# Optimization experiments

Hardware: AMD Instinct MI355X
Metric: run time of the kernel (lower is better)

## Reference

```python
import jax, jax.numpy as jnp
import numpy as np

NUM_HEADS = 8

def setup_inputs() -> dict:
    key = jax.random.key(0)
    ks = jax.random.split(key, 5)
    B, T, N, D = 2, 8, 1024, 512
    x = jax.random.normal(ks[0], (B, T, N, D), dtype=jnp.float32)
    s = 1.0 / np.sqrt(D)
    W_qkv = jax.random.normal(ks[1], (D, 3 * D), dtype=jnp.float32) * s
    b_qkv = jnp.zeros((3 * D,), dtype=jnp.float32)
    W_proj = jax.random.normal(ks[2], (D, D), dtype=jnp.float32) * s
    b_proj = jnp.zeros((D,), dtype=jnp.float32)
    return {"x": x, "W_qkv": W_qkv, "b_qkv": b_qkv, "W_proj": W_proj, "b_proj": b_proj}

def reference(x, W_qkv, b_qkv, W_proj, b_proj):
    B, T, N, D = x.shape
    H = NUM_HEADS
    hd = D // H
    scale = hd ** -0.5
    xf = x.reshape(B * T, N, D)  # fold frames into batch
    qkv = xf @ W_qkv + b_qkv  # (BT, N, 3D)
    qkv = qkv.reshape(B * T, N, 3, H, hd)
    q = qkv[:, :, 0].transpose(0, 2, 1, 3)  # (BT, H, N, hd)
    k = qkv[:, :, 1].transpose(0, 2, 1, 3)
    v = qkv[:, :, 2].transpose(0, 2, 1, 3)
    attn = jnp.einsum('bhnd,bhmd->bhnm', q, k) * scale
    attn = jax.nn.softmax(attn, axis=-1)  # dropout is identity in eval mode
    out = jnp.einsum('bhnm,bhmd->bhnd', attn, v)
    out = out.transpose(0, 2, 1, 3).reshape(B * T, N, D)
    out = out @ W_proj + b_proj
    return out.reshape(B, T, N, D)
```

## Files before the change

### kernel.cpp

```cpp
#include <hip/hip_runtime.h>

typedef __bf16 b16x8 __attribute__((ext_vector_type(8)));
typedef float f32x4 __attribute__((ext_vector_type(4)));
typedef float f32x16 __attribute__((ext_vector_type(16)));
typedef unsigned int u32;

static __device__ __forceinline__ f32x4 mfma16(b16x8 a, b16x8 b, f32x4 c) {
  return __builtin_amdgcn_mfma_f32_16x16x32_bf16(a, b, c, 0, 0, 0);
}
static __device__ __forceinline__ f32x16 mfma32(b16x8 a, b16x8 b, f32x16 c) {
  return __builtin_amdgcn_mfma_f32_32x32x16_bf16(a, b, c, 0, 0, 0);
}

static __device__ __forceinline__ unsigned short f2bf(float f) {
  unsigned u = __builtin_bit_cast(unsigned, f);
  u += 0x7fffu + ((u >> 16) & 1u);
  return (unsigned short)(u >> 16);
}
static __device__ __forceinline__ u32 cvtpk(float lo, float hi) {
  u32 d;
  asm("v_cvt_pk_bf16_f32 %0, %1, %2" : "=v"(d) : "v"(lo), "v"(hi));
  return d;
}
static __device__ __forceinline__ float ex2(float x) {
#if __has_builtin(__builtin_amdgcn_exp2f)
  return __builtin_amdgcn_exp2f(x);
#else
  return exp2f(x);
#endif
}

static __device__ __forceinline__ void gload16(const void* g, void* s) {
  __builtin_amdgcn_global_load_lds((const __attribute__((address_space(1))) void*)g,
                                   (__attribute__((address_space(3))) void*)s, 16, 0, 0);
}

__global__ __launch_bounds__(256) void cvt_x(const float* __restrict__ in,
                                             unsigned short* __restrict__ out, int n8) {
  int i = blockIdx.x * 256 + threadIdx.x;
  if (i >= n8) return;
  const float4* p = (const float4*)in + (size_t)2 * i;
  float4 a = p[0], b = p[1];
  unsigned r0 = f2bf(a.x) | ((unsigned)f2bf(a.y) << 16);
  unsigned r1 = f2bf(a.z) | ((unsigned)f2bf(a.w) << 16);
  unsigned r2 = f2bf(b.x) | ((unsigned)f2bf(b.y) << 16);
  unsigned r3 = f2bf(b.z) | ((unsigned)f2bf(b.w) << 16);
  ((uint4*)out)[i] = make_uint4(r0, r1, r2, r3);
}

__global__ __launch_bounds__(256) void tr_w(const float* __restrict__ in,
                                            unsigned short* __restrict__ out, int R, int C) {
  int idx = blockIdx.x * 256 + threadIdx.x;
  if (idx >= R * C) return;
  int r = idx / C, c = idx % C;
  out[(size_t)c * R + r] = f2bf(in[idx]);
}

template <int MODE>
__global__ __launch_bounds__(256) void gemm_bt_bias(const unsigned short* __restrict__ A,
                                                    const unsigned short* __restrict__ Bt,
                                                    const float* __restrict__ bias,
                                                    void* __restrict__ Cout, int M, int N, int K,
                                                    int nbx) {
  __shared__ unsigned short As[128 * 64];
  __shared__ unsigned short Bs[128 * 64];
  const int tid = threadIdx.x;
  const int w = tid >> 6, l = tid & 63, g = l >> 4, lm = l & 15;
  const int wr = w >> 1, wc = w & 1;
  const int per = gridDim.x >> 3;
  const int wg = (blockIdx.x & 7) * per + (blockIdx.x >> 3);
  const int bm = wg / nbx, bn = wg % nbx;

  f32x4 acc[4][4];
#pragma unroll
  for (int i = 0; i < 4; ++i)
#pragma unroll
    for (int j = 0; j < 4; ++j) acc[i][j] = {0.f, 0.f, 0.f, 0.f};

  const int Kb = K * 2;
  const char* Abase = (const char*)A + (size_t)(bm * 128) * Kb;
  const char* Bbase = (const char*)Bt + (size_t)(bn * 128) * Kb;
  const int lrow = l >> 3;
  const int srccol = ((l & 7) * 16) ^ (((l >> 3) & 7) << 4);

  for (int kt = 0; kt < K; kt += 64) {
#pragma unroll
    for (int i = w; i < 16; i += 4) {
      gload16(Abase + (size_t)(i * 8 + lrow) * Kb + kt * 2 + srccol, As + i * 512);
      gload16(Bbase + (size_t)(i * 8 + lrow) * Kb + kt * 2 + srccol, Bs + i * 512);
    }
    __syncthreads();
#pragma unroll
    for (int ks = 0; ks < 2; ++ks) {
      b16x8 af[4], bf[4];
#pragma unroll
      for (int rt = 0; rt < 4; ++rt) {
        int row = wr * 64 + rt * 16 + lm;
        af[rt] = *(const b16x8*)((const char*)As + row * 128 +
                                 (((ks * 64) + g * 16) ^ ((lm & 7) << 4)));
      }
#pragma unroll
      for (int ct = 0; ct < 4; ++ct) {
        int row = wc * 64 + ct * 16 + lm;
        bf[ct] = *(const b16x8*)((const char*)Bs + row * 128 +
                                 (((ks * 64) + g * 16) ^ ((lm & 7) << 4)));
      }
      __builtin_amdgcn_s_setprio(1);
#pragma unroll
      for (int rt = 0; rt < 4; ++rt)
#pragma unroll
        for (int ct = 0; ct < 4; ++ct) acc[rt][ct] = mfma16(af[rt], bf[ct], acc[rt][ct]);
      __builtin_amdgcn_s_setprio(0);
    }
    __syncthreads();
  }

#pragma unroll
  for (int ct = 0; ct < 4; ++ct) {
    int col = bn * 128 + wc * 64 + ct * 16 + lm;
    float bv = bias[col];
    float sc = (MODE == 1 && col < 512) ? 0.18033688011112042f : 1.0f;
#pragma unroll
    for (int rt = 0; rt < 4; ++rt) {
      int row0 = bm * 128 + wr * 64 + rt * 16 + g * 4;
#pragma unroll
      for (int j = 0; j < 4; ++j) {
        float v = (acc[rt][ct][j] + bv) * sc;
        if (MODE == 2)
          ((float*)Cout)[(size_t)(row0 + j) * N + col] = v;
        else
          ((unsigned short*)Cout)[(size_t)(row0 + j) * N + col] = f2bf(v);
      }
    }
  }
}

__global__ __launch_bounds__(256) void attn_kernel(const unsigned short* __restrict__ qkv,
                                                   unsigned short* __restrict__ out) {
  __shared__ unsigned short Ks[64 * 64];
  __shared__ unsigned short Vt[64 * 64];
  __shared__ unsigned short Ps[4 * 32 * 64];

  const int tid = threadIdx.x;
  const int w = tid >> 6, l = tid & 63, g = l >> 4, lm = l & 15;
  const int lq = l & 31, hi = l >> 5;
  const int id = blockIdx.x;
  const int id2 = (id & 7) * 128 + (id >> 3);
  const int qt = id2 & 7, h = (id2 >> 3) & 7, bt = id2 >> 6;
  const size_t rb = (size_t)bt * 1024;

  const int qrow_sw = qt * 128 + w * 32 + lq;
  b16x8 qf[4];
#pragma unroll
  for (int ks = 0; ks < 4; ++ks)
    qf[ks] = *(const b16x8*)(qkv + (rb + qrow_sw) * 1536 + h * 64 + ks * 16 + hi * 8);

  f32x4 o[2][4];
#pragma unroll
  for (int rt = 0; rt < 2; ++rt)
#pragma unroll
    for (int dt = 0; dt < 4; ++dt) o[rt][dt] = {0.f, 0.f, 0.f, 0.f};
  float la0 = 0.f, la1 = 0.f, la2 = 0.f, la3 = 0.f;

  const int krow_l = l >> 3;
  const int srccol = ((l & 7) * 16) ^ (((l >> 3) & 7) << 4);
  const char* kbase = (const char*)(qkv + rb * 1536 + 512 + (size_t)h * 64);
  const unsigned short* vbase = qkv + rb * 1536 + 1024 + (size_t)h * 64 + w * 16;
  char* Psw = (char*)Ps + w * 4096;

  uint4 va = *(const uint4*)(vbase + (size_t)l * 1536);
  uint4 vb = *(const uint4*)(vbase + (size_t)l * 1536 + 8);

  for (int kb = 0; kb < 16; ++kb) {
    const int k0 = kb * 64;
#pragma unroll
    for (int ii = 0; ii < 2; ++ii) {
      int i = w * 2 + ii;
      gload16(kbase + (size_t)(k0 + i * 8 + krow_l) * 3072 + srccol, Ks + i * 512);
    }
    {
      u32 vv[8] = {va.x, va.y, va.z, va.w, vb.x, vb.y, vb.z, vb.w};
#pragma unroll
      for (int k2 = 0; k2 < 8; ++k2) {
        int d0 = w * 16 + 2 * k2, d1 = d0 + 1;
        *(unsigned short*)((char*)Vt + d0 * 128 + ((2 * l) ^ ((d0 & 7) << 4))) =
            (unsigned short)(vv[k2] & 0xffffu);
        *(unsigned short*)((char*)Vt + d1 * 128 + ((2 * l) ^ ((d1 & 7) << 4))) =
            (unsigned short)(vv[k2] >> 16);
      }
    }
    __syncthreads();

    {
      int kn = ((kb + 1) & 15) * 64;
      va = *(const uint4*)(vbase + (size_t)(kn + l) * 1536);
      vb = *(const uint4*)(vbase + (size_t)(kn + l) * 1536 + 8);
    }

    f32x16 s0 = {0.f, 0.f, 0.f, 0.f, 0.f, 0.f, 0.f, 0.f, 0.f, 0.f, 0.f, 0.f, 0.f, 0.f, 0.f, 0.f};
    f32x16 s1 = s0;
    __builtin_amdgcn_s_setprio(1);
#pragma unroll
    for (int ks = 0; ks < 4; ++ks) {
      int co = (ks * 32 + hi * 16) ^ ((lq & 7) << 4);
      b16x8 k0f = *(const b16x8*)((const char*)Ks + lq * 128 + co);
      b16x8 k1f = *(const b16x8*)((const char*)Ks + (32 + lq) * 128 + co);
      s0 = mfma32(k0f, qf[ks], s0);
      s1 = mfma32(k1f, qf[ks], s1);
    }
    __builtin_amdgcn_s_setprio(0);

#pragma unroll
    for (int r = 0; r < 16; ++r) {
      s0[r] = ex2(s0[r]);
      s1[r] = ex2(s1[r]);
    }
#pragma unroll
    for (int r = 0; r < 16; r += 4) {
      la0 += s0[r]; la1 += s0[r + 1]; la2 += s0[r + 2]; la3 += s0[r + 3];
      la0 += s1[r]; la1 += s1[r + 1]; la2 += s1[r + 2]; la3 += s1[r + 3];
    }

#pragma unroll
    for (int gi = 0; gi < 4; ++gi) {
      int cb = 16 * gi + 8 * hi;
      char* prow = Psw + lq * 128;
      *(uint2*)(prow + (cb ^ ((lq & 7) << 4))) =
          make_uint2(cvtpk(s0[4 * gi], s0[4 * gi + 1]), cvtpk(s0[4 * gi + 2], s0[4 * gi + 3]));
      *(uint2*)(prow + ((64 + cb) ^ ((lq & 7) << 4))) =
          make_uint2(cvtpk(s1[4 * gi], s1[4 * gi + 1]), cvtpk(s1[4 * gi + 2], s1[4 * gi + 3]));
    }

#pragma unroll
    for (int ks = 0; ks < 2; ++ks) {
      b16x8 pa[2];
#pragma unroll
      for (int rt = 0; rt < 2; ++rt) {
        int pr = rt * 16 + lm;
        pa[rt] = *(const b16x8*)(Psw + pr * 128 + (((ks * 64) + g * 16) ^ ((lm & 7) << 4)));
      }
      __builtin_amdgcn_s_setprio(1);
#pragma unroll
      for (int dt = 0; dt < 4; ++dt) {
        int d = dt * 16 + lm;
        b16x8 vf = *(const b16x8*)((const char*)Vt + d * 128 +
                                   (((ks * 64) + g * 16) ^ ((d & 7) << 4)));
        o[0][dt] = mfma16(pa[0], vf, o[0][dt]);
        o[1][dt] = mfma16(pa[1], vf, o[1][dt]);
      }
      __builtin_amdgcn_s_setprio(0);
    }
    __syncthreads();
  }

  float lsum = (la0 + la1) + (la2 + la3);
  lsum += __shfl_xor(lsum, 32);
  float inv = 1.0f / lsum;
#pragma unroll
  for (int rt = 0; rt < 2; ++rt) {
    float i0 = __shfl(inv, rt * 16 + g * 4 + 0);
    float i1 = __shfl(inv, rt * 16 + g * 4 + 1);
    float i2 = __shfl(inv, rt * 16 + g * 4 + 2);
    float i3 = __shfl(inv, rt * 16 + g * 4 + 3);
    float iv[4] = {i0, i1, i2, i3};
#pragma unroll
    for (int dt = 0; dt < 4; ++dt)
#pragma unroll
      for (int j = 0; j < 4; ++j) {
        int nrow = qt * 128 + w * 32 + rt * 16 + g * 4 + j;
        out[(rb + nrow) * 512 + h * 64 + dt * 16 + lm] = f2bf(o[rt][dt][j] * iv[j]);
      }
  }
}

extern "C" void kernel_launch(void* const* d_in, const int* in_sizes, int n_in, void* d_out,
                              int out_size, void* d_ws, size_t ws_size, hipStream_t stream) {
  const float* x = (const float*)d_in[0];
  const float* Wqkv = (const float*)d_in[1];
  const float* bqkv = (const float*)d_in[2];
  const float* Wproj = (const float*)d_in[3];
  const float* bproj = (const float*)d_in[4];
  float* outp = (float*)d_out;

  char* ws = (char*)d_ws;
  unsigned short* xb = (unsigned short*)(ws);
  unsigned short* wqkvT = (unsigned short*)(ws + 16777216);
  unsigned short* wprojT = (unsigned short*)(ws + 18350080);
  unsigned short* qkvb = (unsigned short*)(ws + 18874368);
  unsigned short* attno = (unsigned short*)(ws + 69206016);

  cvt_x<<<4096, 256, 0, stream>>>(x, xb, 1048576);
  tr_w<<<3072, 256, 0, stream>>>(Wqkv, wqkvT, 512, 1536);
  tr_w<<<1024, 256, 0, stream>>>(Wproj, wprojT, 512, 512);
  gemm_bt_bias<1><<<1536, 256, 0, stream>>>(xb, wqkvT, bqkv, qkvb, 16384, 1536, 512, 12);
  attn_kernel<<<1024, 256, 0, stream>>>(qkvb, attno);
  gemm_bt_bias<2><<<512, 256, 0, stream>>>(attno, wprojT, bproj, outp, 16384, 512, 512, 4);
}
```

Baseline: 207.0 us.

## Double attention query tile per wave to reuse K/V tiles across more rows

Each wave now handles 64 query rows instead of 32, so a block covers 256 queries and the grid halves to 512 blocks. Each K/V tile staged in shared memory feeds twice as many MFMAs, halving K/V global loads and LDS staging per query. The cost is higher register pressure (double accumulators and score tiles), a larger P buffer in LDS, and fewer blocks to fill the GPU. A launch_bounds occupancy hint of 2 is added.

```diff
diff --git a/kernel.cpp b/kernel.cpp
--- a/kernel.cpp
+++ b/kernel.cpp
@@ -135,38 +135,41 @@
   }
 }
 
-__global__ __launch_bounds__(256) void attn_kernel(const unsigned short* __restrict__ qkv,
-                                                   unsigned short* __restrict__ out) {
+__global__ __launch_bounds__(256, 2) void attn_kernel(const unsigned short* __restrict__ qkv,
+                                                      unsigned short* __restrict__ out) {
   __shared__ unsigned short Ks[64 * 64];
   __shared__ unsigned short Vt[64 * 64];
-  __shared__ unsigned short Ps[4 * 32 * 64];
+  __shared__ unsigned short Ps[4 * 64 * 64];
 
   const int tid = threadIdx.x;
   const int w = tid >> 6, l = tid & 63, g = l >> 4, lm = l & 15;
   const int lq = l & 31, hi = l >> 5;
   const int id = blockIdx.x;
-  const int id2 = (id & 7) * 128 + (id >> 3);
-  const int qt = id2 & 7, h = (id2 >> 3) & 7, bt = id2 >> 6;
+  const int id2 = (id & 7) * 64 + (id >> 3);
+  const int qt = id2 & 3, h = (id2 >> 2) & 7, bt = id2 >> 5;
   const size_t rb = (size_t)bt * 1024;
-
-  const int qrow_sw = qt * 128 + w * 32 + lq;
-  b16x8 qf[4];
-#pragma unroll
-  for (int ks = 0; ks < 4; ++ks)
-    qf[ks] = *(const b16x8*)(qkv + (rb + qrow_sw) * 1536 + h * 64 + ks * 16 + hi * 8);
-
-  f32x4 o[2][4];
-#pragma unroll
-  for (int rt = 0; rt < 2; ++rt)
+  const int qbase = qt * 256 + w * 64;
+
+  b16x8 qfA[4], qfB[4];
+#pragma unroll
+  for (int ks = 0; ks < 4; ++ks) {
+    qfA[ks] = *(const b16x8*)(qkv + (rb + qbase + lq) * 1536 + h * 64 + ks * 16 + hi * 8);
+    qfB[ks] = *(const b16x8*)(qkv + (rb + qbase + 32 + lq) * 1536 + h * 64 + ks * 16 + hi * 8);
+  }
+
+  f32x4 o[4][4];
+#pragma unroll
+  for (int rt = 0; rt < 4; ++rt)
 #pragma unroll
     for (int dt = 0; dt < 4; ++dt) o[rt][dt] = {0.f, 0.f, 0.f, 0.f};
-  float la0 = 0.f, la1 = 0.f, la2 = 0.f, la3 = 0.f;
+  float laA0 = 0.f, laA1 = 0.f, laA2 = 0.f, laA3 = 0.f;
+  float laB0 = 0.f, laB1 = 0.f, laB2 = 0.f, laB3 = 0.f;
 
   const int krow_l = l >> 3;
   const int srccol = ((l & 7) * 16) ^ (((l >> 3) & 7) << 4);
   const char* kbase = (const char*)(qkv + rb * 1536 + 512 + (size_t)h * 64);
   const unsigned short* vbase = qkv + rb * 1536 + 1024 + (size_t)h * 64 + w * 16;
-  char* Psw = (char*)Ps + w * 4096;
+  char* Psw = (char*)Ps + w * 8192;
 
   uint4 va = *(const uint4*)(vbase + (size_t)l * 1536);
   uint4 vb = *(const uint4*)(vbase + (size_t)l * 1536 + 8);
@@ -197,45 +200,60 @@
       vb = *(const uint4*)(vbase + (size_t)(kn + l) * 1536 + 8);
     }
 
-    f32x16 s0 = {0.f, 0.f, 0.f, 0.f, 0.f, 0.f, 0.f, 0.f, 0.f, 0.f, 0.f, 0.f, 0.f, 0.f, 0.f, 0.f};
-    f32x16 s1 = s0;
+    f32x16 sA0 = {0.f, 0.f, 0.f, 0.f, 0.f, 0.f, 0.f, 0.f, 0.f, 0.f, 0.f, 0.f, 0.f, 0.f, 0.f, 0.f};
+    f32x16 sA1 = sA0, sB0 = sA0, sB1 = sA0;
     __builtin_amdgcn_s_setprio(1);
 #pragma unroll
     for (int ks = 0; ks < 4; ++ks) {
       int co = (ks * 32 + hi * 16) ^ ((lq & 7) << 4);
       b16x8 k0f = *(const b16x8*)((const char*)Ks + lq * 128 + co);
       b16x8 k1f = *(const b16x8*)((const char*)Ks + (32 + lq) * 128 + co);
-      s0 = mfma32(k0f, qf[ks], s0);
-      s1 = mfma32(k1f, qf[ks], s1);
+      sA0 = mfma32(k0f, qfA[ks], sA0);
+      sA1 = mfma32(k1f, qfA[ks], sA1);
+      sB0 = mfma32(k0f, qfB[ks], sB0);
+      sB1 = mfma32(k1f, qfB[ks], sB1);
     }
     __builtin_amdgcn_s_setprio(0);
 
 #pragma unroll
     for (int r = 0; r < 16; ++r) {
-      s0[r] = ex2(s0[r]);
-      s1[r] = ex2(s1[r]);
+      sA0[r] = ex2(sA0[r]);
+      sA1[r] = ex2(sA1[r]);
+      sB0[r] = ex2(sB0[r]);
+      sB1[r] = ex2(sB1[r]);
     }
 #pragma unroll
     for (int r = 0; r < 16; r += 4) {
-      la0 += s0[r]; la1 += s0[r + 1]; la2 += s0[r + 2]; la3 += s0[r + 3];
-      la0 += s1[r]; la1 += s1[r + 1]; la2 += s1[r + 2]; la3 += s1[r + 3];
+      laA0 += sA0[r] + sA1[r];
+      laA1 += sA0[r + 1] + sA1[r + 1];
+      laA2 += sA0[r + 2] + sA1[r + 2];
+      laA3 += sA0[r + 3] + sA1[r + 3];
+      laB0 += sB0[r] + sB1[r];
+      laB1 += sB0[r + 1] + sB1[r + 1];
+      laB2 += sB0[r + 2] + sB1[r + 2];
+      laB3 += sB0[r + 3] + sB1[r + 3];
     }
 
 #pragma unroll
     for (int gi = 0; gi < 4; ++gi) {
       int cb = 16 * gi + 8 * hi;
-      char* prow = Psw + lq * 128;
-      *(uint2*)(prow + (cb ^ ((lq & 7) << 4))) =
-          make_uint2(cvtpk(s0[4 * gi], s0[4 * gi + 1]), cvtpk(s0[4 * gi + 2], s0[4 * gi + 3]));
-      *(uint2*)(prow + ((64 + cb) ^ ((lq & 7) << 4))) =
-          make_uint2(cvtpk(s1[4 * gi], s1[4 * gi + 1]), cvtpk(s1[4 * gi + 2], s1[4 * gi + 3]));
+      char* prowA = Psw + lq * 128;
+      char* prowB = Psw + (32 + lq) * 128;
+      *(uint2*)(prowA + (cb ^ ((lq & 7) << 4))) =
+          make_uint2(cvtpk(sA0[4 * gi], sA0[4 * gi + 1]), cvtpk(sA0[4 * gi + 2], sA0[4 * gi + 3]));
+      *(uint2*)(prowA + ((64 + cb) ^ ((lq & 7) << 4))) =
+          make_uint2(cvtpk(sA1[4 * gi], sA1[4 * gi + 1]), cvtpk(sA1[4 * gi + 2], sA1[4 * gi + 3]));
+      *(uint2*)(prowB + (cb ^ ((lq & 7) << 4))) =
+          make_uint2(cvtpk(sB0[4 * gi], sB0[4 * gi + 1]), cvtpk(sB0[4 * gi + 2], sB0[4 * gi + 3]));
+      *(uint2*)(prowB + ((64 + cb) ^ ((lq & 7) << 4))) =
+          make_uint2(cvtpk(sB1[4 * gi], sB1[4 * gi + 1]), cvtpk(sB1[4 * gi + 2], sB1[4 * gi + 3]));
     }
 
 #pragma unroll
     for (int ks = 0; ks < 2; ++ks) {
-      b16x8 pa[2];
-#pragma unroll
-      for (int rt = 0; rt < 2; ++rt) {
+      b16x8 pa[4];
+#pragma unroll
+      for (int rt = 0; rt < 4; ++rt) {
         int pr = rt * 16 + lm;
         pa[rt] = *(const b16x8*)(Psw + pr * 128 + (((ks * 64) + g * 16) ^ ((lm & 7) << 4)));
       }
@@ -245,29 +263,34 @@
         int d = dt * 16 + lm;
         b16x8 vf = *(const b16x8*)((const char*)Vt + d * 128 +
                                    (((ks * 64) + g * 16) ^ ((d & 7) << 4)));
-        o[0][dt] = mfma16(pa[0], vf, o[0][dt]);
-        o[1][dt] = mfma16(pa[1], vf, o[1][dt]);
+#pragma unroll
+        for (int rt = 0; rt < 4; ++rt) o[rt][dt] = mfma16(pa[rt], vf, o[rt][dt]);
       }
       __builtin_amdgcn_s_setprio(0);
     }
     __syncthreads();
   }
 
-  float lsum = (la0 + la1) + (la2 + la3);
-  lsum += __shfl_xor(lsum, 32);
-  float inv = 1.0f / lsum;
-#pragma unroll
-  for (int rt = 0; rt < 2; ++rt) {
-    float i0 = __shfl(inv, rt * 16 + g * 4 + 0);
-    float i1 = __shfl(inv, rt * 16 + g * 4 + 1);
-    float i2 = __shfl(inv, rt * 16 + g * 4 + 2);
-    float i3 = __shfl(inv, rt * 16 + g * 4 + 3);
+  float lsumA = (laA0 + laA1) + (laA2 + laA3);
+  float lsumB = (laB0 + laB1) + (laB2 + laB3);
+  lsumA += __shfl_xor(lsumA, 32);
+  lsumB += __shfl_xor(lsumB, 32);
+  float invA = 1.0f / lsumA;
+  float invB = 1.0f / lsumB;
+#pragma unroll
+  for (int rt = 0; rt < 4; ++rt) {
+    float src = (rt < 2) ? invA : invB;
+    int lbase = (rt & 1) * 16 + g * 4;
+    float i0 = __shfl(src, lbase + 0);
+    float i1 = __shfl(src, lbase + 1);
+    float i2 = __shfl(src, lbase + 2);
+    float i3 = __shfl(src, lbase + 3);
     float iv[4] = {i0, i1, i2, i3};
 #pragma unroll
     for (int dt = 0; dt < 4; ++dt)
 #pragma unroll
       for (int j = 0; j < 4; ++j) {
-        int nrow = qt * 128 + w * 32 + rt * 16 + g * 4 + j;
+        int nrow = qbase + rt * 16 + g * 4 + j;
         out[(rb + nrow) * 512 + h * 64 + dt * 16 + lm] = f2bf(o[rt][dt][j] * iv[j]);
       }
   }
@@ -293,6 +316,6 @@
   tr_w<<<3072, 256, 0, stream>>>(Wqkv, wqkvT, 512, 1536);
   tr_w<<<1024, 256, 0, stream>>>(Wproj, wprojT, 512, 512);
   gemm_bt_bias<1><<<1536, 256, 0, stream>>>(xb, wqkvT, bqkv, qkvb, 16384, 1536, 512, 12);
-  attn_kernel<<<1024, 256, 0, stream>>>(qkvb, attno);
+  attn_kernel<<<512, 256, 0, stream>>>(qkvb, attno);
   gemm_bt_bias<2><<<512, 256, 0, stream>>>(attno, wprojT, bproj, outp, 16384, 512, 512, 4);
 }
```

After: 206.3 us. No clear change (-0.4%).
